# Optimization experiments

Measured on AMD Instinct MI355X. Metric: run time of the kernel, lower is better.

## Reference

```python
import jax, jax.numpy as jnp
import numpy as np

N_NODES = 50000


def setup_inputs() -> dict:
    key = jax.random.key(0)
    k1, k2, k3, k4, k5, k6 = jax.random.split(key, 6)
    N, E, D, F = 50000, 800000, 512, 256
    feature_ori = jax.random.normal(k1, (N, D), dtype=jnp.float32)
    feature_aug = jax.random.normal(k2, (N, D), dtype=jnp.float32)
    edge_row = jax.random.randint(k3, (E,), 0, N, dtype=jnp.int32)
    edge_col = jax.random.randint(k4, (E,), 0, N, dtype=jnp.int32)
    edge_val = jax.random.uniform(k5, (E,), dtype=jnp.float32)
    # kaiming-uniform-ish init for weight, zeros for bias (as in reset_parameters)
    bound = float(np.sqrt(6.0 / D))
    weight = jax.random.uniform(k6, (D, F), dtype=jnp.float32, minval=-bound, maxval=bound)
    bias = jnp.zeros((F,), dtype=jnp.float32)
    return {
        "feature_ori": feature_ori,
        "feature_aug": feature_aug,
        "edge_row": edge_row,
        "edge_col": edge_col,
        "edge_val": edge_val,
        "weight": weight,
        "bias": bias,
    }


def _branch(feat, weight, bias, edge_row, edge_col, edge_val):
    # support = X @ W  -> [N, F]
    support = feat @ weight
    # sparse aggregation: out[i] = sum_{e: row[e]=i} val[e] * support[col[e]]
    msgs = edge_val[:, None] * support[edge_col]          # [E, F]
    out = jax.ops.segment_sum(msgs, edge_row, num_segments=N_NODES)
    return jax.nn.relu(out + bias)


def reference(feature_ori, feature_aug, edge_row, edge_col, edge_val, weight, bias):
    out_ori = _branch(feature_ori, weight, bias, edge_row, edge_col, edge_val)
    out_aug = _branch(feature_aug, weight, bias, edge_row, edge_col, edge_val)
    return (out_ori, out_aug)
```

## Files before the change

### kernel.cpp

```cpp
#include <hip/hip_runtime.h>
#include <hip/hip_bf16.h>

#define NNODES 50000
#define NEDGES 800000
#define DIN    512
#define FOUT   256

typedef __attribute__((ext_vector_type(8))) short short8;
typedef __attribute__((ext_vector_type(4))) float f32x4;

static __device__ __forceinline__ unsigned short f2bf(float f) {
    unsigned int u = __float_as_uint(f);
    u += 0x7FFF + ((u >> 16) & 1);
    return (unsigned short)(u >> 16);
}
static __device__ __forceinline__ float bf2f(unsigned short h) {
    return __uint_as_float(((unsigned int)h) << 16);
}
static __device__ __forceinline__ unsigned int pk2bf(float a, float b) {
    __hip_bfloat162 h = __float22bfloat162_rn(make_float2(a, b));
    return *(unsigned int*)&h;
}

__global__ void convert_hist(const float* __restrict__ W, unsigned short* __restrict__ Wt,
                             const int* __restrict__ row, int* __restrict__ cnt) {
    int b = blockIdx.x;
    if (b < 512) {
        int o = b * 256 + threadIdx.x;
        int n = o >> 9, k = o & 511;
        Wt[o] = f2bf(W[k * FOUT + n]);
    } else {
        int e = (b - 512) * 256 + threadIdx.x;
        if (e < NEDGES) atomicAdd(&cnt[row[e]], 1);
    }
}

__global__ void scan_partial(const int* __restrict__ cnt, int* __restrict__ partial) {
    __shared__ int sm[256];
    int i = blockIdx.x * 256 + threadIdx.x;
    int v = (i < NNODES) ? cnt[i] : 0;
    sm[threadIdx.x] = v; __syncthreads();
    for (int s = 128; s > 0; s >>= 1) {
        if (threadIdx.x < s) sm[threadIdx.x] += sm[threadIdx.x + s];
        __syncthreads();
    }
    if (threadIdx.x == 0) partial[blockIdx.x] = sm[0];
}

__global__ void scan_exclusive_small(int* __restrict__ partial, int nb) {
    __shared__ int sm[256];
    int t = threadIdx.x;
    int v = (t < nb) ? partial[t] : 0;
    sm[t] = v; __syncthreads();
    for (int off = 1; off < 256; off <<= 1) {
        int add = (t >= off) ? sm[t - off] : 0;
        __syncthreads();
        sm[t] += add;
        __syncthreads();
    }
    if (t < nb) partial[t] = sm[t] - v;
}

__global__ void scan_write(int* __restrict__ cnt, const int* __restrict__ partial,
                           int* __restrict__ row_start) {
    __shared__ int sm[256];
    int t = threadIdx.x;
    int i = blockIdx.x * 256 + t;
    int v = (i < NNODES) ? cnt[i] : 0;
    sm[t] = v; __syncthreads();
    for (int off = 1; off < 256; off <<= 1) {
        int add = (t >= off) ? sm[t - off] : 0;
        __syncthreads();
        sm[t] += add;
        __syncthreads();
    }
    if (i < NNODES) { row_start[i] = partial[blockIdx.x] + sm[t] - v; cnt[i] = 0; }
    if (i == 0) row_start[NNODES] = NEDGES;
}

__global__ void scatter_kernel(const int* __restrict__ row, const int* __restrict__ col,
                               const float* __restrict__ val,
                               const int* __restrict__ row_start,
                               int* __restrict__ cursor, unsigned int* __restrict__ cv) {
    int e = blockIdx.x * 256 + threadIdx.x;
    if (e < NEDGES) {
        int r = row[e];
        int pos = atomicAdd(&cursor[r], 1);
        unsigned int vb = f2bf(val[e]);
        cv[row_start[r] + pos] = (vb << 16) | (unsigned int)col[e];
    }
}

__global__ __launch_bounds__(512, 2)
void gemm_kernel(const float* __restrict__ Xo, const float* __restrict__ Xa,
                 const unsigned short* __restrict__ Wt,
                 unsigned short* __restrict__ S) {
    __shared__ __align__(16) unsigned short As[128][72];
    __shared__ __align__(16) unsigned short Bs[256][72];
    const int tid = threadIdx.x;
    const int branch = blockIdx.z;
    const float* __restrict__ X = branch ? Xa : Xo;
    const int m_base = blockIdx.x * 128;
    const int lane = tid & 63, wave = tid >> 6;
    const int wm = (wave >> 2) * 64, wn = (wave & 3) * 64;
    const int quad = lane >> 4, r16 = lane & 15;

    f32x4 acc[4][4] = {};

    const int scol = (tid & 7) * 8;
    const int srow = tid >> 3;

    float4 a0[2], a1[2];
    uint4  breg[4];

    {
        #pragma unroll
        for (int i = 0; i < 2; i++) {
            int gm = m_base + i * 64 + srow;
            const float* p = &X[(long)gm * DIN + scol];
            bool ok = gm < NNODES;
            a0[i] = ok ? *(const float4*)p       : make_float4(0.f,0.f,0.f,0.f);
            a1[i] = ok ? *(const float4*)(p + 4) : make_float4(0.f,0.f,0.f,0.f);
        }
        #pragma unroll
        for (int i = 0; i < 4; i++)
            breg[i] = *(const uint4*)&Wt[(long)(i * 64 + srow) * DIN + scol];
    }

    for (int k0 = 0; k0 < DIN; k0 += 64) {
        #pragma unroll
        for (int i = 0; i < 2; i++) {
            uint4 h;
            h.x = pk2bf(a0[i].x, a0[i].y);
            h.y = pk2bf(a0[i].z, a0[i].w);
            h.z = pk2bf(a1[i].x, a1[i].y);
            h.w = pk2bf(a1[i].z, a1[i].w);
            *(uint4*)&As[i * 64 + srow][scol] = h;
        }
        #pragma unroll
        for (int i = 0; i < 4; i++)
            *(uint4*)&Bs[i * 64 + srow][scol] = breg[i];
        __syncthreads();

        if (k0 + 64 < DIN) {
            int k1 = k0 + 64;
            #pragma unroll
            for (int i = 0; i < 2; i++) {
                int gm = m_base + i * 64 + srow;
                const float* p = &X[(long)gm * DIN + k1 + scol];
                bool ok = gm < NNODES;
                a0[i] = ok ? *(const float4*)p       : make_float4(0.f,0.f,0.f,0.f);
                a1[i] = ok ? *(const float4*)(p + 4) : make_float4(0.f,0.f,0.f,0.f);
            }
            #pragma unroll
            for (int i = 0; i < 4; i++)
                breg[i] = *(const uint4*)&Wt[(long)(i * 64 + srow) * DIN + k1 + scol];
        }

        #pragma unroll
        for (int w = 0; w < 2; w++) {
            short8 a_frag[4], b_frag[4];
            #pragma unroll
            for (int mi = 0; mi < 4; mi++)
                a_frag[mi] = *(const short8*)&As[wm + mi * 16 + r16][w * 32 + quad * 8];
            #pragma unroll
            for (int ni = 0; ni < 4; ni++)
                b_frag[ni] = *(const short8*)&Bs[wn + ni * 16 + r16][w * 32 + quad * 8];
            #pragma unroll
            for (int mi = 0; mi < 4; mi++)
                #pragma unroll
                for (int ni = 0; ni < 4; ni++)
                    acc[mi][ni] = __builtin_amdgcn_mfma_f32_16x16x32_bf16(
                        a_frag[mi], b_frag[ni], acc[mi][ni], 0, 0, 0);
        }
        __syncthreads();
    }

    #pragma unroll
    for (int mi = 0; mi < 4; mi++) {
        #pragma unroll
        for (int rr = 0; rr < 4; rr++) {
            int m = m_base + wm + mi * 16 + quad * 4 + rr;
            if (m < NNODES) {
                #pragma unroll
                for (int ni = 0; ni < 4; ni++) {
                    int n = wn + ni * 16 + r16;
                    int pos = ((n >> 2) * 8) + branch * 4 + (n & 3);
                    S[(long)m * 512 + pos] = f2bf(acc[mi][ni][rr]);
                }
            }
        }
    }
}

#define ACCUM(p, v) { \
    ao0 += v * __uint_as_float(p.x << 16); ao1 += v * __uint_as_float(p.x & 0xFFFF0000u); \
    ao2 += v * __uint_as_float(p.y << 16); ao3 += v * __uint_as_float(p.y & 0xFFFF0000u); \
    aa0 += v * __uint_as_float(p.z << 16); aa1 += v * __uint_as_float(p.z & 0xFFFF0000u); \
    aa2 += v * __uint_as_float(p.w << 16); aa3 += v * __uint_as_float(p.w & 0xFFFF0000u); }

__global__ __launch_bounds__(256)
void aggregate_kernel(const int* __restrict__ row_start,
                      const unsigned int* __restrict__ cv,
                      const unsigned short* __restrict__ S,
                      const float* __restrict__ bias, float* __restrict__ out) {
    int node = blockIdx.x * 4 + (threadIdx.x >> 6);
    int lane = threadIdx.x & 63;
    if (node >= NNODES) return;
    int s = row_start[node], e = row_start[node + 1];
    float ao0 = 0.f, ao1 = 0.f, ao2 = 0.f, ao3 = 0.f;
    float aa0 = 0.f, aa1 = 0.f, aa2 = 0.f, aa3 = 0.f;
    const long rowoff = (long)lane * 8;

    for (int base = s; base < e; base += 64) {
        int cnt = min(64, e - base);
        unsigned int cvw = (lane < cnt) ? cv[base + lane] : 0u;
        int j = 0;
        for (; j + 4 <= cnt; j += 4) {
            unsigned int w0 = __shfl(cvw, j);
            unsigned int w1 = __shfl(cvw, j + 1);
            unsigned int w2 = __shfl(cvw, j + 2);
            unsigned int w3 = __shfl(cvw, j + 3);
            uint4 p0 = *(const uint4*)&S[(long)(w0 & 0xFFFFu) * 512 + rowoff];
            uint4 p1 = *(const uint4*)&S[(long)(w1 & 0xFFFFu) * 512 + rowoff];
            uint4 p2 = *(const uint4*)&S[(long)(w2 & 0xFFFFu) * 512 + rowoff];
            uint4 p3 = *(const uint4*)&S[(long)(w3 & 0xFFFFu) * 512 + rowoff];
            float v0 = __uint_as_float(w0 & 0xFFFF0000u);
            float v1 = __uint_as_float(w1 & 0xFFFF0000u);
            float v2 = __uint_as_float(w2 & 0xFFFF0000u);
            float v3 = __uint_as_float(w3 & 0xFFFF0000u);
            ACCUM(p0, v0); ACCUM(p1, v1); ACCUM(p2, v2); ACCUM(p3, v3);
        }
        for (; j < cnt; j++) {
            unsigned int w = __shfl(cvw, j);
            uint4 p = *(const uint4*)&S[(long)(w & 0xFFFFu) * 512 + rowoff];
            float v = __uint_as_float(w & 0xFFFF0000u);
            ACCUM(p, v);
        }
    }

    float4 b = *(const float4*)&bias[lane * 4];
    long o = (long)node * FOUT + lane * 4;
    float4 ro, ra;
    ro.x = fmaxf(ao0 + b.x, 0.f); ro.y = fmaxf(ao1 + b.y, 0.f);
    ro.z = fmaxf(ao2 + b.z, 0.f); ro.w = fmaxf(ao3 + b.w, 0.f);
    ra.x = fmaxf(aa0 + b.x, 0.f); ra.y = fmaxf(aa1 + b.y, 0.f);
    ra.z = fmaxf(aa2 + b.z, 0.f); ra.w = fmaxf(aa3 + b.w, 0.f);
    *(float4*)&out[o] = ro;
    *(float4*)&out[(long)NNODES * FOUT + o] = ra;
}

extern "C" void kernel_launch(void* const* d_in, const int* in_sizes, int n_in,
                              void* d_out, int out_size, void* d_ws, size_t ws_size,
                              hipStream_t stream) {
    const float* Xo   = (const float*)d_in[0];
    const float* Xa   = (const float*)d_in[1];
    const int*   erow = (const int*)d_in[2];
    const int*   ecol = (const int*)d_in[3];
    const float* eval_= (const float*)d_in[4];
    const float* W    = (const float*)d_in[5];
    const float* bias = (const float*)d_in[6];
    float* out = (float*)d_out;

    char* ws = (char*)d_ws;
    unsigned short* S         = (unsigned short*)(ws);
    unsigned short* Wt        = (unsigned short*)(ws + 51200000);
    int*            cnt       = (int*)(ws + 51462144);
    int*            row_start = (int*)(ws + 51662144);
    int*            partial   = (int*)(ws + 51862208);
    unsigned int*   cv        = (unsigned int*)(ws + 51863232);

    (void)in_sizes; (void)n_in; (void)out_size; (void)ws_size;

    hipMemsetAsync(cnt, 0, 200000, stream);
    convert_hist<<<512 + 3125, 256, 0, stream>>>(W, Wt, erow, cnt);
    scan_partial<<<196, 256, 0, stream>>>(cnt, partial);
    scan_exclusive_small<<<1, 256, 0, stream>>>(partial, 196);
    scan_write<<<196, 256, 0, stream>>>(cnt, partial, row_start);
    scatter_kernel<<<3125, 256, 0, stream>>>(erow, ecol, eval_, row_start, cnt, cv);

    dim3 gg(391, 1, 2);
    gemm_kernel<<<gg, 512, 0, stream>>>(Xo, Xa, Wt, S);

    aggregate_kernel<<<12500, 256, 0, stream>>>(row_start, cv, S, bias, out);
}
```

Baseline: 536.4 us.

## Fuse both branches in one GEMM block sharing W tiles, relayout S

The GEMM now computes both the original and augmented branches in the same block, so each W tile loaded into shared memory serves two A tiles. The M tile drops to 64 rows and the K step to 32, with no register prefetch, and launch bounds are raised to allow more resident blocks. The interleaved S layout changes to 16-element chunks per branch, and the aggregate kernel's lane mapping and output writes change to match, each lane now covering 8 columns of one branch. Dropping the software prefetch may expose global load latency, which the higher occupancy is meant to hide.

New measurement: 487.0 us. -9.2%, faster.

```diff
diff --git a/kernel.cpp b/kernel.cpp
--- a/kernel.cpp
+++ b/kernel.cpp
@@ -13,9 +13,6 @@
     unsigned int u = __float_as_uint(f);
     u += 0x7FFF + ((u >> 16) & 1);
     return (unsigned short)(u >> 16);
-}
-static __device__ __forceinline__ float bf2f(unsigned short h) {
-    return __uint_as_float(((unsigned int)h) << 16);
 }
 static __device__ __forceinline__ unsigned int pk2bf(float a, float b) {
     __hip_bfloat162 h = __float22bfloat162_rn(make_float2(a, b));
@@ -91,93 +88,69 @@
     }
 }
 
-__global__ __launch_bounds__(512, 2)
+__global__ __launch_bounds__(512, 4)
 void gemm_kernel(const float* __restrict__ Xo, const float* __restrict__ Xa,
                  const unsigned short* __restrict__ Wt,
                  unsigned short* __restrict__ S) {
-    __shared__ __align__(16) unsigned short As[128][72];
-    __shared__ __align__(16) unsigned short Bs[256][72];
+    __shared__ __align__(16) unsigned short Ao[64][40];
+    __shared__ __align__(16) unsigned short Aa[64][40];
+    __shared__ __align__(16) unsigned short Bs[256][40];
     const int tid = threadIdx.x;
-    const int branch = blockIdx.z;
-    const float* __restrict__ X = branch ? Xa : Xo;
-    const int m_base = blockIdx.x * 128;
+    const int m_base = blockIdx.x * 64;
     const int lane = tid & 63, wave = tid >> 6;
-    const int wm = (wave >> 2) * 64, wn = (wave & 3) * 64;
+    const int wm = (wave >> 2) * 32, wn = (wave & 3) * 64;
     const int quad = lane >> 4, r16 = lane & 15;
 
-    f32x4 acc[4][4] = {};
-
-    const int scol = (tid & 7) * 8;
-    const int srow = tid >> 3;
-
-    float4 a0[2], a1[2];
-    uint4  breg[4];
-
-    {
+    f32x4 accO[2][4] = {};
+    f32x4 accA[2][4] = {};
+
+    const int srowA = tid >> 3;
+    const int scolA = (tid & 7) * 4;
+    const int browB = tid >> 2;
+    const int bsegB = (tid & 3) * 8;
+
+    const bool okA = (m_base + srowA) < NNODES;
+    const float* __restrict__ pXo = &Xo[(long)(m_base + srowA) * DIN + scolA];
+    const float* __restrict__ pXa = &Xa[(long)(m_base + srowA) * DIN + scolA];
+
+    for (int k0 = 0; k0 < DIN; k0 += 32) {
+        float4 vo = okA ? *(const float4*)(pXo + k0) : make_float4(0.f,0.f,0.f,0.f);
+        float4 va = okA ? *(const float4*)(pXa + k0) : make_float4(0.f,0.f,0.f,0.f);
+        uint2 ho, ha;
+        ho.x = pk2bf(vo.x, vo.y); ho.y = pk2bf(vo.z, vo.w);
+        ha.x = pk2bf(va.x, va.y); ha.y = pk2bf(va.z, va.w);
+        *(uint2*)&Ao[srowA][scolA] = ho;
+        *(uint2*)&Aa[srowA][scolA] = ha;
         #pragma unroll
         for (int i = 0; i < 2; i++) {
-            int gm = m_base + i * 64 + srow;
-            const float* p = &X[(long)gm * DIN + scol];
-            bool ok = gm < NNODES;
-            a0[i] = ok ? *(const float4*)p       : make_float4(0.f,0.f,0.f,0.f);
-            a1[i] = ok ? *(const float4*)(p + 4) : make_float4(0.f,0.f,0.f,0.f);
-        }
-        #pragma unroll
-        for (int i = 0; i < 4; i++)
-            breg[i] = *(const uint4*)&Wt[(long)(i * 64 + srow) * DIN + scol];
-    }
-
-    for (int k0 = 0; k0 < DIN; k0 += 64) {
-        #pragma unroll
-        for (int i = 0; i < 2; i++) {
-            uint4 h;
-            h.x = pk2bf(a0[i].x, a0[i].y);
-            h.y = pk2bf(a0[i].z, a0[i].w);
-            h.z = pk2bf(a1[i].x, a1[i].y);
-            h.w = pk2bf(a1[i].z, a1[i].w);
-            *(uint4*)&As[i * 64 + srow][scol] = h;
-        }
-        #pragma unroll
-        for (int i = 0; i < 4; i++)
-            *(uint4*)&Bs[i * 64 + srow][scol] = breg[i];
-        __syncthreads();
-
-        if (k0 + 64 < DIN) {
-            int k1 = k0 + 64;
+            int row = i * 128 + browB;
+            *(uint4*)&Bs[row][bsegB] = *(const uint4*)&Wt[(long)row * DIN + k0 + bsegB];
+        }
+        __syncthreads();
+
+        short8 b_frag[4], aO[2], aA[2];
+        #pragma unroll
+        for (int ni = 0; ni < 4; ni++)
+            b_frag[ni] = *(const short8*)&Bs[wn + ni * 16 + r16][quad * 8];
+        #pragma unroll
+        for (int mi = 0; mi < 2; mi++) {
+            aO[mi] = *(const short8*)&Ao[wm + mi * 16 + r16][quad * 8];
+            aA[mi] = *(const short8*)&Aa[wm + mi * 16 + r16][quad * 8];
+        }
+        #pragma unroll
+        for (int mi = 0; mi < 2; mi++)
             #pragma unroll
-            for (int i = 0; i < 2; i++) {
-                int gm = m_base + i * 64 + srow;
-                const float* p = &X[(long)gm * DIN + k1 + scol];
-                bool ok = gm < NNODES;
-                a0[i] = ok ? *(const float4*)p       : make_float4(0.f,0.f,0.f,0.f);
-                a1[i] = ok ? *(const float4*)(p + 4) : make_float4(0.f,0.f,0.f,0.f);
+            for (int ni = 0; ni < 4; ni++) {
+                accO[mi][ni] = __builtin_amdgcn_mfma_f32_16x16x32_bf16(
+                    aO[mi], b_frag[ni], accO[mi][ni], 0, 0, 0);
+                accA[mi][ni] = __builtin_amdgcn_mfma_f32_16x16x32_bf16(
+                    aA[mi], b_frag[ni], accA[mi][ni], 0, 0, 0);
             }
-            #pragma unroll
-            for (int i = 0; i < 4; i++)
-                breg[i] = *(const uint4*)&Wt[(long)(i * 64 + srow) * DIN + k1 + scol];
-        }
-
-        #pragma unroll
-        for (int w = 0; w < 2; w++) {
-            short8 a_frag[4], b_frag[4];
-            #pragma unroll
-            for (int mi = 0; mi < 4; mi++)
-                a_frag[mi] = *(const short8*)&As[wm + mi * 16 + r16][w * 32 + quad * 8];
-            #pragma unroll
-            for (int ni = 0; ni < 4; ni++)
-                b_frag[ni] = *(const short8*)&Bs[wn + ni * 16 + r16][w * 32 + quad * 8];
-            #pragma unroll
-            for (int mi = 0; mi < 4; mi++)
-                #pragma unroll
-                for (int ni = 0; ni < 4; ni++)
-                    acc[mi][ni] = __builtin_amdgcn_mfma_f32_16x16x32_bf16(
-                        a_frag[mi], b_frag[ni], acc[mi][ni], 0, 0, 0);
-        }
         __syncthreads();
     }
 
     #pragma unroll
-    for (int mi = 0; mi < 4; mi++) {
+    for (int mi = 0; mi < 2; mi++) {
         #pragma unroll
         for (int rr = 0; rr < 4; rr++) {
             int m = m_base + wm + mi * 16 + quad * 4 + rr;
@@ -185,19 +158,20 @@
                 #pragma unroll
                 for (int ni = 0; ni < 4; ni++) {
                     int n = wn + ni * 16 + r16;
-                    int pos = ((n >> 2) * 8) + branch * 4 + (n & 3);
-                    S[(long)m * 512 + pos] = f2bf(acc[mi][ni][rr]);
+                    long base = (long)m * 512 + ((n >> 4) * 32) + (n & 15);
+                    S[base]      = f2bf(accO[mi][ni][rr]);
+                    S[base + 16] = f2bf(accA[mi][ni][rr]);
                 }
             }
         }
     }
 }
 
-#define ACCUM(p, v) { \
-    ao0 += v * __uint_as_float(p.x << 16); ao1 += v * __uint_as_float(p.x & 0xFFFF0000u); \
-    ao2 += v * __uint_as_float(p.y << 16); ao3 += v * __uint_as_float(p.y & 0xFFFF0000u); \
-    aa0 += v * __uint_as_float(p.z << 16); aa1 += v * __uint_as_float(p.z & 0xFFFF0000u); \
-    aa2 += v * __uint_as_float(p.w << 16); aa3 += v * __uint_as_float(p.w & 0xFFFF0000u); }
+#define ACC8(p, v) { \
+    f0 += v * __uint_as_float(p.x << 16); f1 += v * __uint_as_float(p.x & 0xFFFF0000u); \
+    f2 += v * __uint_as_float(p.y << 16); f3 += v * __uint_as_float(p.y & 0xFFFF0000u); \
+    f4 += v * __uint_as_float(p.z << 16); f5 += v * __uint_as_float(p.z & 0xFFFF0000u); \
+    f6 += v * __uint_as_float(p.w << 16); f7 += v * __uint_as_float(p.w & 0xFFFF0000u); }
 
 __global__ __launch_bounds__(256)
 void aggregate_kernel(const int* __restrict__ row_start,
@@ -208,9 +182,9 @@
     int lane = threadIdx.x & 63;
     if (node >= NNODES) return;
     int s = row_start[node], e = row_start[node + 1];
-    float ao0 = 0.f, ao1 = 0.f, ao2 = 0.f, ao3 = 0.f;
-    float aa0 = 0.f, aa1 = 0.f, aa2 = 0.f, aa3 = 0.f;
-    const long rowoff = (long)lane * 8;
+    float f0=0.f,f1=0.f,f2=0.f,f3=0.f,f4=0.f,f5=0.f,f6=0.f,f7=0.f;
+    const int l = lane & 31, b = lane >> 5;
+    const long rowoff = (long)((l >> 1) * 32 + b * 16 + (l & 1) * 8);
 
     for (int base = s; base < e; base += 64) {
         int cnt = min(64, e - base);
@@ -229,25 +203,27 @@
             float v1 = __uint_as_float(w1 & 0xFFFF0000u);
             float v2 = __uint_as_float(w2 & 0xFFFF0000u);
             float v3 = __uint_as_float(w3 & 0xFFFF0000u);
-            ACCUM(p0, v0); ACCUM(p1, v1); ACCUM(p2, v2); ACCUM(p3, v3);
+            ACC8(p0, v0); ACC8(p1, v1); ACC8(p2, v2); ACC8(p3, v3);
         }
         for (; j < cnt; j++) {
             unsigned int w = __shfl(cvw, j);
             uint4 p = *(const uint4*)&S[(long)(w & 0xFFFFu) * 512 + rowoff];
             float v = __uint_as_float(w & 0xFFFF0000u);
-            ACCUM(p, v);
-        }
-    }
-
-    float4 b = *(const float4*)&bias[lane * 4];
-    long o = (long)node * FOUT + lane * 4;
-    float4 ro, ra;
-    ro.x = fmaxf(ao0 + b.x, 0.f); ro.y = fmaxf(ao1 + b.y, 0.f);
-    ro.z = fmaxf(ao2 + b.z, 0.f); ro.w = fmaxf(ao3 + b.w, 0.f);
-    ra.x = fmaxf(aa0 + b.x, 0.f); ra.y = fmaxf(aa1 + b.y, 0.f);
-    ra.z = fmaxf(aa2 + b.z, 0.f); ra.w = fmaxf(aa3 + b.w, 0.f);
-    *(float4*)&out[o] = ro;
-    *(float4*)&out[(long)NNODES * FOUT + o] = ra;
+            ACC8(p, v);
+        }
+    }
+
+    const float* bp = &bias[l * 8];
+    float4 b0 = *(const float4*)bp;
+    float4 b1 = *(const float4*)(bp + 4);
+    long o = (long)b * NNODES * FOUT + (long)node * FOUT + l * 8;
+    float4 r0, r1;
+    r0.x = fmaxf(f0 + b0.x, 0.f); r0.y = fmaxf(f1 + b0.y, 0.f);
+    r0.z = fmaxf(f2 + b0.z, 0.f); r0.w = fmaxf(f3 + b0.w, 0.f);
+    r1.x = fmaxf(f4 + b1.x, 0.f); r1.y = fmaxf(f5 + b1.y, 0.f);
+    r1.z = fmaxf(f6 + b1.z, 0.f); r1.w = fmaxf(f7 + b1.w, 0.f);
+    *(float4*)&out[o] = r0;
+    *(float4*)&out[o + 4] = r1;
 }
 
 extern "C" void kernel_launch(void* const* d_in, const int* in_sizes, int n_in,
@@ -279,8 +255,7 @@
     scan_write<<<196, 256, 0, stream>>>(cnt, partial, row_start);
     scatter_kernel<<<3125, 256, 0, stream>>>(erow, ecol, eval_, row_start, cnt, cv);
 
-    dim3 gg(391, 1, 2);
-    gemm_kernel<<<gg, 512, 0, stream>>>(Xo, Xa, Wt, S);
+    gemm_kernel<<<782, 512, 0, stream>>>(Xo, Xa, Wt, S);
 
     aggregate_kernel<<<12500, 256, 0, stream>>>(row_start, cv, S, bias, out);
 }
```
